# Kernel tuning notes

Hardware: AMD Instinct MI355X
Metric: run time of the kernel (lower is better)

## Reference

```python
import jax, jax.numpy as jnp
import numpy as np

B, C, H, W_ = 256, 512, 28, 28
D = H * W_


def setup_inputs() -> dict:
    key = jax.random.key(0)
    k1, k2, k3 = jax.random.split(key, 3)
    x = jax.random.normal(k1, (B, C, H, W_), dtype=jnp.float32)
    # Per-channel Linear(D -> 1): weight [C, D], bias [C]
    W = jax.random.normal(k2, (C, D), dtype=jnp.float32) * (1.0 / np.sqrt(D))
    b = jax.random.normal(k3, (C,), dtype=jnp.float32) * 0.01
    return {"x": x, "W": W, "b": b}


def reference(x, W, b):
    # x: [B, C, H, W] -> [B, C, D]; per-channel dot product with W[c] + b[c]
    xf = x.reshape(x.shape[0], x.shape[1], -1)
    out = jnp.einsum("bcd,cd->bc", xf, W) + b  # [B, C]
    return out[..., None]  # [B, C, 1] matching torch.cat(dim=1) of (B,1,1) slices
```

## Files before the change

### kernel.cpp

```cpp
#include <hip/hip_runtime.h>
#include <hip/hip_bf16.h>


#define B_ 256
#define C_ 512
#define D_ 784
#define D4 (D_ / 4)

__global__ __launch_bounds__(256) void dot_rows_kernel(
    const float* __restrict__ x,
    const float* __restrict__ W,
    const float* __restrict__ bias,
    float* __restrict__ out)
{
    const int wave = (int)((blockIdx.x * (unsigned)blockDim.x + threadIdx.x) >> 6);
    const int lane = threadIdx.x & 63;
    if (wave >= B_ * C_) return;

    const int c = wave & (C_ - 1);

    const float4* __restrict__ xr = reinterpret_cast<const float4*>(x + (size_t)wave * D_);
    const float4* __restrict__ wr = reinterpret_cast<const float4*>(W + (size_t)c * D_);

    float sum = 0.0f;
    #pragma unroll
    for (int i = lane; i < D4; i += 64) {
        float4 xv = xr[i];
        float4 wv = wr[i];
        sum += xv.x * wv.x + xv.y * wv.y + xv.z * wv.z + xv.w * wv.w;
    }

    #pragma unroll
    for (int off = 32; off > 0; off >>= 1)
        sum += __shfl_down(sum, off, 64);

    if (lane == 0)
        out[wave] = sum + bias[c];
}

extern "C" void kernel_launch(void* const* d_in, const int* in_sizes, int n_in,
                              void* d_out, int out_size, void* d_ws, size_t ws_size,
                              hipStream_t stream) {
    const float* x    = (const float*)d_in[0];
    const float* W    = (const float*)d_in[1];
    const float* bias = (const float*)d_in[2];
    float* out        = (float*)d_out;

    const int total_waves = B_ * C_;
    const int waves_per_block = 256 / 64;
    const int grid = total_waves / waves_per_block;

    dot_rows_kernel<<<grid, 256, 0, stream>>>(x, W, bias, out);
}
```

Before: 78.18 us.

## Reuse per-channel weight row across eight batch rows per wave with nontemporal x loads

Each wave now holds the weight row for one channel in registers and processes eight batch rows, so W is read once per eight dot products instead of once each. The loop over the row is fully unrolled into four float4 loads per row, and the x loads use nontemporal hints because x is streamed once. This cuts the grid by eight, and more loads are in flight per wave at the cost of more registers. The kernel remains bound by streaming x (about 411MB), so the effect depends on whether W traffic or cache contention was limiting bandwidth.

```diff
diff --git a/kernel.cpp b/kernel.cpp
--- a/kernel.cpp
+++ b/kernel.cpp
@@ -5,7 +5,10 @@
 #define B_ 256
 #define C_ 512
 #define D_ 784
-#define D4 (D_ / 4)
+#define D4 196
+#define R_ 8
+
+typedef float f32x4 __attribute__((ext_vector_type(4)));
 
 __global__ __launch_bounds__(256) void dot_rows_kernel(
     const float* __restrict__ x,
@@ -13,29 +16,53 @@
     const float* __restrict__ bias,
     float* __restrict__ out)
 {
-    const int wave = (int)((blockIdx.x * (unsigned)blockDim.x + threadIdx.x) >> 6);
+    const int wid  = (int)(blockIdx.x * 4u + (threadIdx.x >> 6));
     const int lane = threadIdx.x & 63;
-    if (wave >= B_ * C_) return;
 
-    const int c = wave & (C_ - 1);
+    const int c  = wid & (C_ - 1);
+    const int b0 = (wid >> 9) * R_;
 
-    const float4* __restrict__ xr = reinterpret_cast<const float4*>(x + (size_t)wave * D_);
-    const float4* __restrict__ wr = reinterpret_cast<const float4*>(W + (size_t)c * D_);
+    const f32x4* __restrict__ wr = reinterpret_cast<const f32x4*>(W + (size_t)c * D_);
+    const f32x4 w0 = wr[lane];
+    const f32x4 w1 = wr[lane + 64];
+    const f32x4 w2 = wr[lane + 128];
+    f32x4 w3 = (f32x4)(0.f);
+    if (lane < (D4 - 192)) w3 = wr[lane + 192];
 
-    float sum = 0.0f;
+    float s[R_];
     #pragma unroll
-    for (int i = lane; i < D4; i += 64) {
-        float4 xv = xr[i];
-        float4 wv = wr[i];
-        sum += xv.x * wv.x + xv.y * wv.y + xv.z * wv.z + xv.w * wv.w;
+    for (int r = 0; r < R_; ++r) {
+        const f32x4* __restrict__ xr =
+            reinterpret_cast<const f32x4*>(x + ((size_t)(b0 + r) * C_ + c) * D_);
+        const f32x4 x0 = __builtin_nontemporal_load(xr + lane);
+        const f32x4 x1 = __builtin_nontemporal_load(xr + lane + 64);
+        const f32x4 x2 = __builtin_nontemporal_load(xr + lane + 128);
+        f32x4 x3 = (f32x4)(0.f);
+        if (lane < (D4 - 192)) x3 = __builtin_nontemporal_load(xr + lane + 192);
+
+        float acc;
+        acc  = x0.x * w0.x + x0.y * w0.y + x0.z * w0.z + x0.w * w0.w;
+        acc += x1.x * w1.x + x1.y * w1.y + x1.z * w1.z + x1.w * w1.w;
+        acc += x2.x * w2.x + x2.y * w2.y + x2.z * w2.z + x2.w * w2.w;
+        acc += x3.x * w3.x + x3.y * w3.y + x3.z * w3.z + x3.w * w3.w;
+        s[r] = acc;
     }
 
     #pragma unroll
-    for (int off = 32; off > 0; off >>= 1)
-        sum += __shfl_down(sum, off, 64);
+    for (int r = 0; r < R_; ++r) {
+        float v = s[r];
+        #pragma unroll
+        for (int off = 32; off > 0; off >>= 1)
+            v += __shfl_down(v, off, 64);
+        s[r] = v;
+    }
 
-    if (lane == 0)
-        out[wave] = sum + bias[c];
+    if (lane == 0) {
+        const float bc = bias[c];
+        #pragma unroll
+        for (int r = 0; r < R_; ++r)
+            out[(size_t)(b0 + r) * C_ + c] = s[r] + bc;
+    }
 }
 
 extern "C" void kernel_launch(void* const* d_in, const int* in_sizes, int n_in,
@@ -46,9 +73,8 @@
     const float* bias = (const float*)d_in[2];
     float* out        = (float*)d_out;
 
-    const int total_waves = B_ * C_;
-    const int waves_per_block = 256 / 64;
-    const int grid = total_waves / waves_per_block;
+    const int total_waves = (B_ / R_) * C_;
+    const int grid = total_waves / 4;
 
     dot_rows_kernel<<<grid, 256, 0, stream>>>(x, W, bias, out);
 }
```

Result: faster. 65.47 us (-16.3%).
